# Kernel optimization log

Hardware: AMD Instinct MI355X
Metric: run time of the kernel (lower is better)

## Reference

```python
import jax, jax.numpy as jnp
import numpy as np

N_NODES = 100_000
N_EDGES = 1_600_000
N_FEAT = 64
E_FEAT = 32
OUT_FEAT = 64


def _xavier_normal(key, shape, gain):
    fan_out, fan_in = shape
    std = gain * np.sqrt(2.0 / (fan_in + fan_out))
    return jax.random.normal(key, shape, dtype=jnp.float32) * std


def setup_inputs() -> dict:
    key = jax.random.key(0)
    ks = jax.random.split(key, 9)
    d_cat = 2 * N_FEAT + E_FEAT  # 160
    n_feat = jax.random.normal(ks[0], (N_NODES, N_FEAT), dtype=jnp.float32)
    e_feat = jax.random.normal(ks[1], (N_EDGES, E_FEAT), dtype=jnp.float32)
    src = jax.random.randint(ks[2], (N_EDGES,), 0, N_NODES, dtype=jnp.int32)
    dst = jax.random.randint(ks[3], (N_EDGES,), 0, N_NODES, dtype=jnp.int32)
    gain = np.sqrt(2.0)
    bound_msg = 1.0 / np.sqrt(d_cat)
    return {
        "n_feat": n_feat,
        "e_feat": e_feat,
        "src": src,
        "dst": dst,
        # W_msg uses default torch Linear init (kaiming-uniform-ish); exact init irrelevant for correctness
        "W_msg_w": jax.random.uniform(ks[4], (OUT_FEAT, d_cat), jnp.float32, -bound_msg, bound_msg),
        "W_msg_b": jax.random.uniform(ks[5], (OUT_FEAT,), jnp.float32, -bound_msg, bound_msg),
        # W uses xavier_normal with gain sqrt(2)
        "W_w": _xavier_normal(ks[6], (2 * OUT_FEAT, d_cat), gain),
        "W_b": jax.random.uniform(ks[7], (2 * OUT_FEAT,), jnp.float32, -bound_msg, bound_msg),
        "a": _xavier_normal(ks[8], (2 * OUT_FEAT, 1), gain),
    }


def reference(n_feat, e_feat, src, dst, W_msg_w, W_msg_b, W_w, W_b, a):
    # gather: per-edge concat [E, 2*n_feat + e_feat]
    feat_cat = jnp.concatenate([n_feat[src], n_feat[dst], e_feat], axis=1)
    # edge attention logits: leaky_relu((feat_cat @ W^T + b) @ a)  -> [E]
    w_feat = feat_cat @ W_w.T + W_b                      # [E, 2*out_feat]
    logits = jax.nn.leaky_relu(w_feat @ a[:, 0])         # [E]
    # edge softmax grouped by destination node
    seg_max = jax.ops.segment_max(logits, dst, num_segments=N_NODES)  # [N]
    ex = jnp.exp(logits - seg_max[dst])                  # [E]
    seg_sum = jax.ops.segment_sum(ex, dst, num_segments=N_NODES)     # [N]
    att = ex / seg_sum[dst]                              # [E]
    # messages and weighted scatter-sum aggregation
    msg = feat_cat @ W_msg_w.T + W_msg_b                 # [E, out_feat]
    agg = jax.ops.segment_sum(att[:, None] * msg, dst, num_segments=N_NODES)  # [N, out_feat]
    return jax.nn.relu(agg)
```

## Files before the change

kernel.cpp:

```cpp
#include <hip/hip_runtime.h>
#include <hip/hip_bf16.h>

#define N_NODES 100000
#define N_EDGES 1600000
#define NF 64
#define EF 32

#define SCAN_B 512
#define SCAN_NB ((N_NODES + SCAN_B - 1) / SCAN_B)

__global__ __launch_bounds__(256) void k0_prep(
    const float* __restrict__ Ww, const float* __restrict__ Wb,
    const float* __restrict__ a, const float* __restrict__ Wmsg,
    float* __restrict__ v, float* __restrict__ W1T, float* __restrict__ W2T,
    float* __restrict__ WmeT) {
  int t = threadIdx.x;
  for (int j = t; j < 160; j += 256) {
    float s = 0.f;
    for (int k = 0; k < 128; ++k) s = fmaf(a[k], Ww[k * 160 + j], s);
    v[j] = s;
  }
  if (t == 0) {
    float s = 0.f;
    for (int k = 0; k < 128; ++k) s = fmaf(a[k], Wb[k], s);
    v[160] = s;
  }
  for (int idx = t; idx < 64 * 64; idx += 256) {
    int j = idx >> 6, i = idx & 63;
    W1T[idx] = Wmsg[i * 160 + j];
    W2T[idx] = Wmsg[i * 160 + 64 + j];
  }
  for (int idx = t; idx < 32 * 64; idx += 256) {
    int j = idx >> 6, i = idx & 63;
    WmeT[idx] = Wmsg[i * 160 + 128 + j];
  }
}

__global__ __launch_bounds__(256) void k1_node(
    const float* __restrict__ nf_g, const float* __restrict__ v,
    const float* __restrict__ W1T, const float* __restrict__ W2T,
    float* __restrict__ s1, float* __restrict__ s2,
    float* __restrict__ m_src, float* __restrict__ m_dst) {
  int n = blockIdx.x * 256 + threadIdx.x;
  if (n >= N_NODES) return;
  const float4* nf4 = (const float4*)(nf_g + (size_t)n * NF);
  float acc[64];
#pragma unroll
  for (int i = 0; i < 64; ++i) acc[i] = 0.f;
  float s1a = 0.f, s2a = 0.f;
  for (int j4 = 0; j4 < 16; ++j4) {
    float4 q = nf4[j4];
    float xs[4] = {q.x, q.y, q.z, q.w};
#pragma unroll
    for (int u = 0; u < 4; ++u) {
      int j = j4 * 4 + u;
      float x = xs[u];
      s1a = fmaf(v[j], x, s1a);
      s2a = fmaf(v[64 + j], x, s2a);
      const float* w = W1T + j * 64;
#pragma unroll
      for (int i = 0; i < 64; ++i) acc[i] = fmaf(w[i], x, acc[i]);
    }
  }
  s1[n] = s1a;
  s2[n] = s2a;
  float* ms = m_src + (size_t)n * NF;
#pragma unroll
  for (int i = 0; i < 64; ++i) ms[i] = acc[i];
#pragma unroll
  for (int i = 0; i < 64; ++i) acc[i] = 0.f;
  for (int j4 = 0; j4 < 16; ++j4) {
    float4 q = nf4[j4];
    float xs[4] = {q.x, q.y, q.z, q.w};
#pragma unroll
    for (int u = 0; u < 4; ++u) {
      int j = j4 * 4 + u;
      float x = xs[u];
      const float* w = W2T + j * 64;
#pragma unroll
      for (int i = 0; i < 64; ++i) acc[i] = fmaf(w[i], x, acc[i]);
    }
  }
  float* md = m_dst + (size_t)n * NF;
#pragma unroll
  for (int i = 0; i < 64; ++i) md[i] = acc[i];
}

__global__ __launch_bounds__(256) void kE_edge(
    const int* __restrict__ src, const int* __restrict__ dst,
    const float* __restrict__ e_feat, const float* __restrict__ s1,
    const float* __restrict__ s2, const float* __restrict__ v,
    float* __restrict__ ex_out, int* __restrict__ cnt) {
  int e = blockIdx.x * 256 + threadIdx.x;
  if (e >= N_EDGES) return;
  int sn = src[e], dn = dst[e];
  const float4* efr = (const float4*)(e_feat + (size_t)e * EF);
  float t = 0.f;
#pragma unroll
  for (int i = 0; i < 8; ++i) {
    float4 q = efr[i];
    t = fmaf(q.x, v[128 + i * 4 + 0], t);
    t = fmaf(q.y, v[128 + i * 4 + 1], t);
    t = fmaf(q.z, v[128 + i * 4 + 2], t);
    t = fmaf(q.w, v[128 + i * 4 + 3], t);
  }
  float lg = s1[sn] + s2[dn] + t + v[160];
  float l = lg > 0.f ? lg : 0.01f * lg;
  ex_out[e] = __expf(l);
  atomicAdd(&cnt[dn], 1);
}

__global__ __launch_bounds__(SCAN_B) void kS1(const int* __restrict__ cnt,
                                              int* __restrict__ bsum) {
  __shared__ int sh[SCAN_B];
  int t = threadIdx.x;
  int i = blockIdx.x * SCAN_B + t;
  sh[t] = (i < N_NODES) ? cnt[i] : 0;
  __syncthreads();
  for (int d = SCAN_B / 2; d > 0; d >>= 1) {
    if (t < d) sh[t] += sh[t + d];
    __syncthreads();
  }
  if (t == 0) bsum[blockIdx.x] = sh[0];
}

__global__ __launch_bounds__(256) void kS2(const int* __restrict__ bsum,
                                           int* __restrict__ boff,
                                           int* __restrict__ row_ptr) {
  __shared__ int sh[256];
  int t = threadIdx.x;
  sh[t] = (t < SCAN_NB) ? bsum[t] : 0;
  __syncthreads();
  for (int d = 1; d < 256; d <<= 1) {
    int val = (t >= d) ? sh[t - d] : 0;
    __syncthreads();
    sh[t] += val;
    __syncthreads();
  }
  if (t < SCAN_NB) boff[t] = (t == 0) ? 0 : sh[t - 1];
  if (t == 255) row_ptr[N_NODES] = sh[255];
}

__global__ __launch_bounds__(SCAN_B) void kS3(const int* __restrict__ cnt,
                                              const int* __restrict__ boff,
                                              int* __restrict__ row_ptr,
                                              int* __restrict__ cursor) {
  __shared__ int sh[SCAN_B];
  int t = threadIdx.x;
  int i = blockIdx.x * SCAN_B + t;
  int val = (i < N_NODES) ? cnt[i] : 0;
  sh[t] = val;
  __syncthreads();
  for (int d = 1; d < SCAN_B; d <<= 1) {
    int u = (t >= d) ? sh[t - d] : 0;
    __syncthreads();
    sh[t] += u;
    __syncthreads();
  }
  if (i < N_NODES) {
    int excl = boff[blockIdx.x] + sh[t] - val;
    row_ptr[i] = excl;
    cursor[i] = excl;
  }
}

__global__ __launch_bounds__(256) void k2_scatter(
    const int* __restrict__ dst, const int* __restrict__ src,
    const float* __restrict__ ex, int* __restrict__ cursor,
    int4* __restrict__ edata) {
  int e = blockIdx.x * 256 + threadIdx.x;
  if (e < N_EDGES) {
    int dn = dst[e];
    int p = atomicAdd(&cursor[dn], 1);
    edata[p] = make_int4(e, src[e], __float_as_int(ex[e]), 0);
  }
}

__global__ __launch_bounds__(256) void k3_agg(
    const int* __restrict__ row_ptr, const int4* __restrict__ edata,
    const float* __restrict__ e_feat, const float* __restrict__ m_src,
    const float* __restrict__ m_dst, const float* __restrict__ WmeT,
    const float* __restrict__ Wmsg_b, float* __restrict__ out) {
  int lane = threadIdx.x & 63;
  int wid = threadIdx.x >> 6;
  int n = blockIdx.x * 4 + wid;
  if (n >= N_NODES) return;
  int start = row_ptr[n];
  int end = row_ptr[n + 1];
  float sum_ex = 0.f, acc_ms = 0.f, acc_ef = 0.f;
  for (int base = start; base < end; base += 64) {
    int4 md = make_int4(0, 0, 0, 0);
    if (base + lane < end) md = edata[base + lane];
    int m = end - base;
    if (m > 64) m = 64;
    int mm4 = (m + 3) & ~3;
    for (int k = 0; k < mm4; k += 4) {
      int ek[4], sk[4];
      float exk[4], efk[4], msk[4];
#pragma unroll
      for (int u = 0; u < 4; ++u) {
        ek[u] = __shfl(md.x, k + u);
        sk[u] = __shfl(md.y, k + u);
        exk[u] = __int_as_float(__shfl(md.z, k + u));
      }
#pragma unroll
      for (int u = 0; u < 4; ++u) {
        efk[u] = e_feat[(size_t)ek[u] * EF + (lane & 31)];
        msk[u] = m_src[(size_t)sk[u] * NF + lane];
      }
#pragma unroll
      for (int u = 0; u < 4; ++u) {
        sum_ex += exk[u];
        acc_ms = fmaf(exk[u], msk[u], acc_ms);
        acc_ef = fmaf(exk[u], efk[u], acc_ef);
      }
    }
  }
  float mm = 0.f;
#pragma unroll
  for (int j = 0; j < 32; ++j) {
    float efj = __shfl(acc_ef, j);
    mm = fmaf(WmeT[j * 64 + lane], efj, mm);
  }
  float o = 0.f;
  if (sum_ex > 0.f) {
    o = (acc_ms + mm) / sum_ex + m_dst[(size_t)n * NF + lane] + Wmsg_b[lane];
    o = fmaxf(o, 0.f);
  }
  out[(size_t)n * NF + lane] = o;
}

extern "C" void kernel_launch(void* const* d_in, const int* in_sizes, int n_in,
                              void* d_out, int out_size, void* d_ws,
                              size_t ws_size, hipStream_t stream) {
  const float* n_feat = (const float*)d_in[0];
  const float* e_feat = (const float*)d_in[1];
  const int* src = (const int*)d_in[2];
  const int* dst = (const int*)d_in[3];
  const float* Wmsg_w = (const float*)d_in[4];
  const float* Wmsg_b = (const float*)d_in[5];
  const float* W_w = (const float*)d_in[6];
  const float* W_b = (const float*)d_in[7];
  const float* a = (const float*)d_in[8];
  float* out = (float*)d_out;

  char* ws = (char*)d_ws;
  size_t off = 0;
  auto alloc = [&](size_t bytes) -> char* {
    char* p = ws + off;
    off = (off + bytes + 255) & ~(size_t)255;
    return p;
  };
  float* v = (float*)alloc(161 * 4);
  float* W1T = (float*)alloc(64 * 64 * 4);
  float* W2T = (float*)alloc(64 * 64 * 4);
  float* WmeT = (float*)alloc(32 * 64 * 4);
  float* s1 = (float*)alloc(N_NODES * 4);
  float* s2 = (float*)alloc(N_NODES * 4);
  float* m_src = (float*)alloc((size_t)N_NODES * NF * 4);
  float* m_dst = (float*)alloc((size_t)N_NODES * NF * 4);
  int* cnt = (int*)alloc(N_NODES * 4);
  int* row_ptr = (int*)alloc((N_NODES + 1) * 4);
  int* cursor = (int*)alloc(N_NODES * 4);
  int* bsum = (int*)alloc(SCAN_NB * 4);
  int* boff = (int*)alloc(SCAN_NB * 4);
  float* ex = (float*)alloc((size_t)N_EDGES * 4);
  int4* edata = (int4*)alloc((size_t)N_EDGES * 16);
  if (off > ws_size) return;

  k0_prep<<<1, 256, 0, stream>>>(W_w, W_b, a, Wmsg_w, v, W1T, W2T, WmeT);
  k1_node<<<(N_NODES + 255) / 256, 256, 0, stream>>>(n_feat, v, W1T, W2T, s1,
                                                     s2, m_src, m_dst);
  hipMemsetAsync(cnt, 0, N_NODES * 4, stream);
  kE_edge<<<(N_EDGES + 255) / 256, 256, 0, stream>>>(src, dst, e_feat, s1, s2,
                                                     v, ex, cnt);
  kS1<<<SCAN_NB, SCAN_B, 0, stream>>>(cnt, bsum);
  kS2<<<1, 256, 0, stream>>>(bsum, boff, row_ptr);
  kS3<<<SCAN_NB, SCAN_B, 0, stream>>>(cnt, boff, row_ptr, cursor);
  k2_scatter<<<(N_EDGES + 255) / 256, 256, 0, stream>>>(dst, src, ex, cursor,
                                                        edata);
  k3_agg<<<(N_NODES + 3) / 4, 256, 0, stream>>>(row_ptr, edata, e_feat, m_src,
                                                m_dst, WmeT, Wmsg_b, out);
}
```

Baseline: 637.0 us.

## Fuse logit computation into CSR scatter, pack edge records into 64 bits

Splits edge counting into a lightweight count kernel and fuses the logit/exp computation into the scatter kernel. This removes the intermediate ex array round-trip. Edge records are packed into 64 bits (21-bit edge id, 17-bit source id, truncated exp value), halving the scatter write and aggregation read traffic. The aggregation kernel now lets the two half-waves fetch e_feat rows for different edges, so each wave covers two edges per e_feat load, and the halves are combined afterwards. The truncated exponent mantissa reduces precision, and the bit widths assume the current node and edge counts.

```diff
diff --git a/kernel.cpp b/kernel.cpp
--- a/kernel.cpp
+++ b/kernel.cpp
@@ -8,6 +8,7 @@
 
 #define SCAN_B 512
 #define SCAN_NB ((N_NODES + SCAN_B - 1) / SCAN_B)
+
 
 __global__ __launch_bounds__(256) void k0_prep(
     const float* __restrict__ Ww, const float* __restrict__ Wb,
@@ -86,11 +87,71 @@
   for (int i = 0; i < 64; ++i) md[i] = acc[i];
 }
 
-__global__ __launch_bounds__(256) void kE_edge(
+__global__ __launch_bounds__(256) void k_count(const int* __restrict__ dst,
+                                               int* __restrict__ cnt) {
+  int e = blockIdx.x * 256 + threadIdx.x;
+  if (e < N_EDGES) atomicAdd(&cnt[dst[e]], 1);
+}
+
+__global__ __launch_bounds__(SCAN_B) void kS1(const int* __restrict__ cnt,
+                                              int* __restrict__ bsum) {
+  __shared__ int sh[SCAN_B];
+  int t = threadIdx.x;
+  int i = blockIdx.x * SCAN_B + t;
+  sh[t] = (i < N_NODES) ? cnt[i] : 0;
+  __syncthreads();
+  for (int d = SCAN_B / 2; d > 0; d >>= 1) {
+    if (t < d) sh[t] += sh[t + d];
+    __syncthreads();
+  }
+  if (t == 0) bsum[blockIdx.x] = sh[0];
+}
+
+__global__ __launch_bounds__(256) void kS2(const int* __restrict__ bsum,
+                                           int* __restrict__ boff,
+                                           int* __restrict__ row_ptr) {
+  __shared__ int sh[256];
+  int t = threadIdx.x;
+  sh[t] = (t < SCAN_NB) ? bsum[t] : 0;
+  __syncthreads();
+  for (int d = 1; d < 256; d <<= 1) {
+    int val = (t >= d) ? sh[t - d] : 0;
+    __syncthreads();
+    sh[t] += val;
+    __syncthreads();
+  }
+  if (t < SCAN_NB) boff[t] = (t == 0) ? 0 : sh[t - 1];
+  if (t == 255) row_ptr[N_NODES] = sh[255];
+}
+
+__global__ __launch_bounds__(SCAN_B) void kS3(const int* __restrict__ cnt,
+                                              const int* __restrict__ boff,
+                                              int* __restrict__ row_ptr,
+                                              int* __restrict__ cursor) {
+  __shared__ int sh[SCAN_B];
+  int t = threadIdx.x;
+  int i = blockIdx.x * SCAN_B + t;
+  int val = (i < N_NODES) ? cnt[i] : 0;
+  sh[t] = val;
+  __syncthreads();
+  for (int d = 1; d < SCAN_B; d <<= 1) {
+    int u = (t >= d) ? sh[t - d] : 0;
+    __syncthreads();
+    sh[t] += u;
+    __syncthreads();
+  }
+  if (i < N_NODES) {
+    int excl = boff[blockIdx.x] + sh[t] - val;
+    row_ptr[i] = excl;
+    cursor[i] = excl;
+  }
+}
+
+__global__ __launch_bounds__(256) void kE_scatter(
     const int* __restrict__ src, const int* __restrict__ dst,
     const float* __restrict__ e_feat, const float* __restrict__ s1,
     const float* __restrict__ s2, const float* __restrict__ v,
-    float* __restrict__ ex_out, int* __restrict__ cnt) {
+    int* __restrict__ cursor, unsigned long long* __restrict__ edata) {
   int e = blockIdx.x * 256 + threadIdx.x;
   if (e >= N_EDGES) return;
   int sn = src[e], dn = dst[e];
@@ -106,78 +167,16 @@
   }
   float lg = s1[sn] + s2[dn] + t + v[160];
   float l = lg > 0.f ? lg : 0.01f * lg;
-  ex_out[e] = __expf(l);
-  atomicAdd(&cnt[dn], 1);
-}
-
-__global__ __launch_bounds__(SCAN_B) void kS1(const int* __restrict__ cnt,
-                                              int* __restrict__ bsum) {
-  __shared__ int sh[SCAN_B];
-  int t = threadIdx.x;
-  int i = blockIdx.x * SCAN_B + t;
-  sh[t] = (i < N_NODES) ? cnt[i] : 0;
-  __syncthreads();
-  for (int d = SCAN_B / 2; d > 0; d >>= 1) {
-    if (t < d) sh[t] += sh[t + d];
-    __syncthreads();
-  }
-  if (t == 0) bsum[blockIdx.x] = sh[0];
-}
-
-__global__ __launch_bounds__(256) void kS2(const int* __restrict__ bsum,
-                                           int* __restrict__ boff,
-                                           int* __restrict__ row_ptr) {
-  __shared__ int sh[256];
-  int t = threadIdx.x;
-  sh[t] = (t < SCAN_NB) ? bsum[t] : 0;
-  __syncthreads();
-  for (int d = 1; d < 256; d <<= 1) {
-    int val = (t >= d) ? sh[t - d] : 0;
-    __syncthreads();
-    sh[t] += val;
-    __syncthreads();
-  }
-  if (t < SCAN_NB) boff[t] = (t == 0) ? 0 : sh[t - 1];
-  if (t == 255) row_ptr[N_NODES] = sh[255];
-}
-
-__global__ __launch_bounds__(SCAN_B) void kS3(const int* __restrict__ cnt,
-                                              const int* __restrict__ boff,
-                                              int* __restrict__ row_ptr,
-                                              int* __restrict__ cursor) {
-  __shared__ int sh[SCAN_B];
-  int t = threadIdx.x;
-  int i = blockIdx.x * SCAN_B + t;
-  int val = (i < N_NODES) ? cnt[i] : 0;
-  sh[t] = val;
-  __syncthreads();
-  for (int d = 1; d < SCAN_B; d <<= 1) {
-    int u = (t >= d) ? sh[t - d] : 0;
-    __syncthreads();
-    sh[t] += u;
-    __syncthreads();
-  }
-  if (i < N_NODES) {
-    int excl = boff[blockIdx.x] + sh[t] - val;
-    row_ptr[i] = excl;
-    cursor[i] = excl;
-  }
-}
-
-__global__ __launch_bounds__(256) void k2_scatter(
-    const int* __restrict__ dst, const int* __restrict__ src,
-    const float* __restrict__ ex, int* __restrict__ cursor,
-    int4* __restrict__ edata) {
-  int e = blockIdx.x * 256 + threadIdx.x;
-  if (e < N_EDGES) {
-    int dn = dst[e];
-    int p = atomicAdd(&cursor[dn], 1);
-    edata[p] = make_int4(e, src[e], __float_as_int(ex[e]), 0);
-  }
+  float ex = __expf(l);
+  int p = atomicAdd(&cursor[dn], 1);
+  unsigned long long pk = ((unsigned long long)(unsigned)e << 43) |
+                          ((unsigned long long)(unsigned)sn << 26) |
+                          (unsigned long long)(__float_as_uint(ex) >> 6);
+  edata[p] = pk;
 }
 
 __global__ __launch_bounds__(256) void k3_agg(
-    const int* __restrict__ row_ptr, const int4* __restrict__ edata,
+    const int* __restrict__ row_ptr, const int2* __restrict__ edata,
     const float* __restrict__ e_feat, const float* __restrict__ m_src,
     const float* __restrict__ m_dst, const float* __restrict__ WmeT,
     const float* __restrict__ Wmsg_b, float* __restrict__ out) {
@@ -187,39 +186,48 @@
   if (n >= N_NODES) return;
   int start = row_ptr[n];
   int end = row_ptr[n + 1];
+  int half = lane >> 5;
+  int col = lane & 31;
   float sum_ex = 0.f, acc_ms = 0.f, acc_ef = 0.f;
   for (int base = start; base < end; base += 64) {
-    int4 md = make_int4(0, 0, 0, 0);
+    int2 md = make_int2(0, 0);
     if (base + lane < end) md = edata[base + lane];
     int m = end - base;
     if (m > 64) m = 64;
     int mm4 = (m + 3) & ~3;
     for (int k = 0; k < mm4; k += 4) {
       int ek[4], sk[4];
-      float exk[4], efk[4], msk[4];
+      float exk[4], msk[4], efh[2], exh[2];
 #pragma unroll
       for (int u = 0; u < 4; ++u) {
-        ek[u] = __shfl(md.x, k + u);
-        sk[u] = __shfl(md.y, k + u);
-        exk[u] = __int_as_float(__shfl(md.z, k + u));
+        unsigned lo = (unsigned)__shfl(md.x, k + u);
+        unsigned hi = (unsigned)__shfl(md.y, k + u);
+        ek[u] = (int)(hi >> 11);
+        sk[u] = (int)(((hi & 0x7FFu) << 6) | (lo >> 26));
+        exk[u] = __uint_as_float((lo & 0x3FFFFFFu) << 6);
       }
-#pragma unroll
-      for (int u = 0; u < 4; ++u) {
-        efk[u] = e_feat[(size_t)ek[u] * EF + (lane & 31)];
+      int eh0 = half ? ek[1] : ek[0];
+      int eh1 = half ? ek[3] : ek[2];
+      exh[0] = half ? exk[1] : exk[0];
+      exh[1] = half ? exk[3] : exk[2];
+#pragma unroll
+      for (int u = 0; u < 4; ++u)
         msk[u] = m_src[(size_t)sk[u] * NF + lane];
-      }
+      efh[0] = e_feat[(size_t)eh0 * EF + col];
+      efh[1] = e_feat[(size_t)eh1 * EF + col];
 #pragma unroll
       for (int u = 0; u < 4; ++u) {
         sum_ex += exk[u];
         acc_ms = fmaf(exk[u], msk[u], acc_ms);
-        acc_ef = fmaf(exk[u], efk[u], acc_ef);
       }
+      acc_ef = fmaf(exh[0], efh[0], acc_ef);
+      acc_ef = fmaf(exh[1], efh[1], acc_ef);
     }
   }
   float mm = 0.f;
 #pragma unroll
   for (int j = 0; j < 32; ++j) {
-    float efj = __shfl(acc_ef, j);
+    float efj = __shfl(acc_ef, j) + __shfl(acc_ef, j + 32);
     mm = fmaf(WmeT[j * 64 + lane], efj, mm);
   }
   float o = 0.f;
@@ -264,21 +272,20 @@
   int* cursor = (int*)alloc(N_NODES * 4);
   int* bsum = (int*)alloc(SCAN_NB * 4);
   int* boff = (int*)alloc(SCAN_NB * 4);
-  float* ex = (float*)alloc((size_t)N_EDGES * 4);
-  int4* edata = (int4*)alloc((size_t)N_EDGES * 16);
+  unsigned long long* edata = (unsigned long long*)alloc((size_t)N_EDGES * 8);
   if (off > ws_size) return;
 
   k0_prep<<<1, 256, 0, stream>>>(W_w, W_b, a, Wmsg_w, v, W1T, W2T, WmeT);
   k1_node<<<(N_NODES + 255) / 256, 256, 0, stream>>>(n_feat, v, W1T, W2T, s1,
                                                      s2, m_src, m_dst);
   hipMemsetAsync(cnt, 0, N_NODES * 4, stream);
-  kE_edge<<<(N_EDGES + 255) / 256, 256, 0, stream>>>(src, dst, e_feat, s1, s2,
-                                                     v, ex, cnt);
+  k_count<<<(N_EDGES + 255) / 256, 256, 0, stream>>>(dst, cnt);
   kS1<<<SCAN_NB, SCAN_B, 0, stream>>>(cnt, bsum);
   kS2<<<1, 256, 0, stream>>>(bsum, boff, row_ptr);
   kS3<<<SCAN_NB, SCAN_B, 0, stream>>>(cnt, boff, row_ptr, cursor);
-  k2_scatter<<<(N_EDGES + 255) / 256, 256, 0, stream>>>(dst, src, ex, cursor,
-                                                        edata);
-  k3_agg<<<(N_NODES + 3) / 4, 256, 0, stream>>>(row_ptr, edata, e_feat, m_src,
-                                                m_dst, WmeT, Wmsg_b, out);
-}
+  kE_scatter<<<(N_EDGES + 255) / 256, 256, 0, stream>>>(src, dst, e_feat, s1,
+                                                        s2, v, cursor, edata);
+  k3_agg<<<(N_NODES + 3) / 4, 256, 0, stream>>>(row_ptr, (const int2*)edata,
+                                                e_feat, m_src, m_dst, WmeT,
+                                                Wmsg_b, out);
+}
```

Result: no change. 627.7 us (-1.5%).
